# Kernel optimization log

Hardware: AMD Instinct MI355X
Metric: run time of the kernel (lower is better)

Reference implementation:

```python
import jax, jax.numpy as jnp
import numpy as np

NB_HEAD = 16
SIZE_PER_HEAD = 64
D_MODEL = 1024
OUT_DIM = NB_HEAD * SIZE_PER_HEAD
BIG_NEG = 1e10


def setup_inputs() -> dict:
    key = jax.random.key(0)
    ks = jax.random.split(key, 6)
    B, L = 2, 2048
    q = jax.random.normal(ks[0], (B, L, D_MODEL), dtype=jnp.float32)
    k = jax.random.normal(ks[1], (B, L, D_MODEL), dtype=jnp.float32)
    v = jax.random.normal(ks[2], (B, L, D_MODEL), dtype=jnp.float32)
    v_mask = jnp.ones((B, L), dtype=jnp.float32)
    q_mask = jnp.ones((B, L), dtype=jnp.float32)
    # glorot_normal-ish init for the three projection kernels
    std = (2.0 / (D_MODEL + OUT_DIM)) ** 0.5
    q_kernel = jax.random.normal(ks[3], (D_MODEL, OUT_DIM), dtype=jnp.float32) * std
    k_kernel = jax.random.normal(ks[4], (D_MODEL, OUT_DIM), dtype=jnp.float32) * std
    v_kernel = jax.random.normal(ks[5], (D_MODEL, OUT_DIM), dtype=jnp.float32) * std
    return {"q": q, "k": k, "v": v, "v_mask": v_mask, "q_mask": q_mask,
            "q_kernel": q_kernel, "k_kernel": k_kernel, "v_kernel": v_kernel}


def reference(q, k, v, v_mask, q_mask, q_kernel, k_kernel, v_kernel):
    B, Lq, _ = q.shape
    Lk = k.shape[1]
    H, D = NB_HEAD, SIZE_PER_HEAD
    # projections -> [B, L, H, D]
    qw = (q @ q_kernel).reshape(B, Lq, H, D)
    kw = (k @ k_kernel).reshape(B, Lk, H, D)
    vw = (v @ v_kernel).reshape(B, Lk, H, D)
    # scaled dot-product scores [B, H, Lq, Lk]
    scores = jnp.einsum('bqhd,bkhd->bhqk', qw, kw) / jnp.sqrt(jnp.float32(D))
    # additive key mask (original permutes so mask broadcasts over key axis)
    scores = scores - (1.0 - v_mask)[:, None, None, :] * BIG_NEG
    a = jax.nn.softmax(scores, axis=-1)
    # weighted sum -> [B, Lq, H, D] -> [B, Lq, H*D]
    o = jnp.einsum('bhqk,bkhd->bqhd', a, vw).reshape(B, Lq, H * D)
    # multiplicative query mask on output
    o = o * q_mask[:, :, None]
    return o
```

## Files before the change

kernel.cpp:

```cpp
#include <hip/hip_runtime.h>
#include <hip/hip_bf16.h>

#define B_SZ 2
#define SEQ  2048
#define DM   1024
#define NH   16
#define HD   64

typedef __attribute__((ext_vector_type(8))) short bf16x8;
typedef __attribute__((ext_vector_type(4))) short bf16x4;
typedef __attribute__((ext_vector_type(4))) float f32x4;
typedef __attribute__((ext_vector_type(16))) float f32x16;

__device__ __forceinline__ short f2b(float f) {
    __hip_bfloat16 h = __float2bfloat16(f);
    return *reinterpret_cast<short*>(&h);
}

__device__ __forceinline__ void async_copy16(void* lds, const void* g) {
    __builtin_amdgcn_global_load_lds(
        (const __attribute__((address_space(1))) void*)g,
        (__attribute__((address_space(3))) void*)lds, 16, 0, 0);
}

__global__ __launch_bounds__(256) void kPre(
    const float* __restrict__ q, const float* __restrict__ k, const float* __restrict__ v,
    const float* __restrict__ w0, const float* __restrict__ w1, const float* __restrict__ w2,
    short* __restrict__ qb, short* __restrict__ kb, short* __restrict__ vb,
    short* __restrict__ t0, short* __restrict__ t1, short* __restrict__ t2) {
    int z = blockIdx.z, tid = threadIdx.x;
    if (z < 3) {
        const float* src = z == 0 ? q : (z == 1 ? k : v);
        short*       dst = z == 0 ? qb : (z == 1 ? kb : vb);
        size_t i = ((size_t)blockIdx.x * 256 + tid) * 8;
        float4 a0 = *reinterpret_cast<const float4*>(src + i);
        float4 a1 = *reinterpret_cast<const float4*>(src + i + 4);
        bf16x8 c;
        c[0] = f2b(a0.x); c[1] = f2b(a0.y); c[2] = f2b(a0.z); c[3] = f2b(a0.w);
        c[4] = f2b(a1.x); c[5] = f2b(a1.y); c[6] = f2b(a1.z); c[7] = f2b(a1.w);
        *reinterpret_cast<bf16x8*>(dst + i) = c;
    } else {
        if (blockIdx.x >= 256) return;
        const float* w = z == 3 ? w0 : (z == 4 ? w1 : w2);
        short*       t = z == 3 ? t0 : (z == 4 ? t1 : t2);
        __shared__ float tile[64][65];
        int n0 = (blockIdx.x & 15) * 64, k0 = (blockIdx.x >> 4) * 64;
        int c = tid & 63, rr = tid >> 6;
#pragma unroll
        for (int i = 0; i < 16; i++) {
            int kk = i * 4 + rr;
            tile[kk][c] = w[(size_t)(k0 + kk) * DM + n0 + c];
        }
        __syncthreads();
#pragma unroll
        for (int i = 0; i < 16; i++) {
            int nn = i * 4 + rr;
            t[(size_t)(n0 + nn) * DM + k0 + c] = f2b(tile[c][nn]);
        }
    }
}

__global__ __launch_bounds__(256) void kProj(
    const short* __restrict__ qb, const short* __restrict__ kb, const short* __restrict__ vb,
    const short* __restrict__ wtq, const short* __restrict__ wtk, const short* __restrict__ wtv,
    short* __restrict__ qw, short* __restrict__ kw, short* __restrict__ vwT) {
    int z = blockIdx.z;
    const short* A  = z == 0 ? qb : (z == 1 ? kb : vb);
    const short* Bt = z == 0 ? wtq : (z == 1 ? wtk : wtv);

    __shared__ short As[128 * 64];
    __shared__ short Bs[128 * 64];

    int tid = threadIdx.x;
    int m0 = blockIdx.y * 128, n0 = blockIdx.x * 128;
    int wv = tid >> 6, lane = tid & 63, quad = lane >> 4, ln = lane & 15;
    int rblk = (wv >> 1) * 64, cblk = (wv & 1) * 64;

    int rA = wv * 32;
    int srow = rA + (lane >> 3), scol = (lane & 7) * 8;

    f32x4 zero = {0.f, 0.f, 0.f, 0.f};
    f32x4 acc[4][4];
#pragma unroll
    for (int rt = 0; rt < 4; rt++)
#pragma unroll
        for (int ct = 0; ct < 4; ct++) acc[rt][ct] = zero;

    for (int ks = 0; ks < DM; ks += 64) {
        const short* gA = A  + (size_t)(m0 + srow) * DM + ks + scol;
        const short* gB = Bt + (size_t)(n0 + srow) * DM + ks + scol;
#pragma unroll
        for (int i = 0; i < 4; i++) {
            async_copy16(&As[(rA + i * 8) * 64], gA + (size_t)i * 8 * DM);
            async_copy16(&Bs[(rA + i * 8) * 64], gB + (size_t)i * 8 * DM);
        }
        __syncthreads();
#pragma unroll
        for (int kc = 0; kc < 2; kc++) {
            bf16x8 af[4], bfv[4];
#pragma unroll
            for (int rt = 0; rt < 4; rt++)
                af[rt] = *reinterpret_cast<bf16x8*>(&As[(rblk + rt * 16 + ln) * 64 + kc * 32 + quad * 8]);
#pragma unroll
            for (int ct = 0; ct < 4; ct++)
                bfv[ct] = *reinterpret_cast<bf16x8*>(&Bs[(cblk + ct * 16 + ln) * 64 + kc * 32 + quad * 8]);
#pragma unroll
            for (int rt = 0; rt < 4; rt++)
#pragma unroll
                for (int ct = 0; ct < 4; ct++)
                    acc[rt][ct] = __builtin_amdgcn_mfma_f32_16x16x32_bf16(
                        af[rt], bfv[ct], acc[rt][ct], 0, 0, 0);
        }
        __syncthreads();
    }

    if (z < 2) {
        short* C = z == 0 ? qw : kw;
#pragma unroll
        for (int rt = 0; rt < 4; rt++)
#pragma unroll
            for (int r = 0; r < 4; r++) {
                int row = m0 + rblk + rt * 16 + quad * 4 + r;
#pragma unroll
                for (int ct = 0; ct < 4; ct++)
                    C[(size_t)row * DM + n0 + cblk + ct * 16 + ln] = f2b(acc[rt][ct][r]);
            }
    } else {
#pragma unroll
        for (int rt = 0; rt < 4; rt++) {
            int srow0 = m0 + rblk + rt * 16 + quad * 4;
            int bb = srow0 >> 11, lk = srow0 & (SEQ - 1);
#pragma unroll
            for (int ct = 0; ct < 4; ct++) {
                int coln = n0 + cblk + ct * 16 + ln;
                int hh = coln >> 6, dd = coln & 63;
                bf16x4 pk;
                pk[0] = f2b(acc[rt][ct][0]); pk[1] = f2b(acc[rt][ct][1]);
                pk[2] = f2b(acc[rt][ct][2]); pk[3] = f2b(acc[rt][ct][3]);
                *reinterpret_cast<bf16x4*>(
                    &vwT[(((size_t)bb * NH + hh) * HD + dd) * SEQ + lk]) = pk;
            }
        }
    }
}

__global__ __launch_bounds__(256, 2) void kAttn(
    const short* __restrict__ qw, const short* __restrict__ kw, const short* __restrict__ vwT,
    const float* __restrict__ vmask, const float* __restrict__ qmask, float* __restrict__ out) {
    int b = blockIdx.z, h = blockIdx.y, lq0 = blockIdx.x * 128;
    int tid = threadIdx.x, wv = tid >> 6, lane = tid & 63;
    int l5 = lane & 31, half = lane >> 5;

    __shared__ short Ks[128][72];
    __shared__ short Vt[64][136];
    __shared__ short Ps[4][32][136];

    const short* qrow = qw + (size_t)(b * SEQ + lq0 + wv * 32 + l5) * DM + h * HD;
    bf16x8 qf[4];
#pragma unroll
    for (int ki = 0; ki < 4; ki++)
        qf[ki] = *reinterpret_cast<const bf16x8*>(qrow + ki * 16 + half * 8);

    float lrow = 0.f;
    f32x16 o0, o1;
#pragma unroll
    for (int i = 0; i < 16; i++) { o0[i] = 0.f; o1[i] = 0.f; }

    int krow = tid >> 1, kcol = (tid & 1) * 32;
    int vrow = tid >> 2, vcol = (tid & 3) * 32;
    const short* kp = kw + (size_t)(b * SEQ + krow) * DM + h * HD + kcol;
    const short* vp = vwT + ((size_t)(b * NH + h) * HD + vrow) * SEQ + vcol;
    const float* vmb = vmask + b * SEQ;

    bf16x8 kr[4], vr[4];
#pragma unroll
    for (int i = 0; i < 4; i++) {
        kr[i] = *reinterpret_cast<const bf16x8*>(kp + i * 8);
        vr[i] = *reinterpret_cast<const bf16x8*>(vp + i * 8);
    }

    for (int it = 0; it < SEQ / 128; it++) {
        int lk0 = it * 128;
#pragma unroll
        for (int i = 0; i < 4; i++) {
            *reinterpret_cast<bf16x8*>(&Ks[krow][kcol + i * 8]) = kr[i];
            *reinterpret_cast<bf16x8*>(&Vt[vrow][vcol + i * 8]) = vr[i];
        }
        __syncthreads();

        if (it + 1 < SEQ / 128) {
            kp += (size_t)128 * DM;
            vp += 128;
#pragma unroll
            for (int i = 0; i < 4; i++) {
                kr[i] = *reinterpret_cast<const bf16x8*>(kp + i * 8);
                vr[i] = *reinterpret_cast<const bf16x8*>(vp + i * 8);
            }
        }

        f32x16 s[4];
#pragma unroll
        for (int lt = 0; lt < 4; lt++)
#pragma unroll
            for (int i = 0; i < 16; i++) s[lt][i] = 0.f;
#pragma unroll
        for (int lt = 0; lt < 4; lt++)
#pragma unroll
            for (int ki = 0; ki < 4; ki++) {
                bf16x8 kf = *reinterpret_cast<bf16x8*>(&Ks[lt * 32 + l5][ki * 16 + half * 8]);
                s[lt] = __builtin_amdgcn_mfma_f32_32x32x16_bf16(kf, qf[ki], s[lt], 0, 0, 0);
            }

        float rs = 0.f;
#pragma unroll
        for (int lt = 0; lt < 4; lt++)
#pragma unroll
            for (int g = 0; g < 4; g++) {
                float4 mv = *reinterpret_cast<const float4*>(
                    &vmb[lk0 + lt * 32 + 8 * g + 4 * half]);
                float p0 = __expf(s[lt][4 * g + 0] * 0.125f - (1.0f - mv.x) * 1e10f);
                float p1 = __expf(s[lt][4 * g + 1] * 0.125f - (1.0f - mv.y) * 1e10f);
                float p2 = __expf(s[lt][4 * g + 2] * 0.125f - (1.0f - mv.z) * 1e10f);
                float p3 = __expf(s[lt][4 * g + 3] * 0.125f - (1.0f - mv.w) * 1e10f);
                rs += (p0 + p1) + (p2 + p3);
                bf16x4 pk;
                pk[0] = f2b(p0); pk[1] = f2b(p1); pk[2] = f2b(p2); pk[3] = f2b(p3);
                *reinterpret_cast<bf16x4*>(&Ps[wv][l5][lt * 32 + 8 * g + 4 * half]) = pk;
            }
        rs += __shfl_xor(rs, 32);
        lrow += rs;

        bf16x8 pf[8];
#pragma unroll
        for (int ki = 0; ki < 8; ki++)
            pf[ki] = *reinterpret_cast<bf16x8*>(&Ps[wv][l5][ki * 16 + half * 8]);

#pragma unroll
        for (int ki = 0; ki < 8; ki++) {
            bf16x8 vf0 = *reinterpret_cast<bf16x8*>(&Vt[l5][ki * 16 + half * 8]);
            bf16x8 vf1 = *reinterpret_cast<bf16x8*>(&Vt[32 + l5][ki * 16 + half * 8]);
            o0 = __builtin_amdgcn_mfma_f32_32x32x16_bf16(vf0, pf[ki], o0, 0, 0, 0);
            o1 = __builtin_amdgcn_mfma_f32_32x32x16_bf16(vf1, pf[ki], o1, 0, 0, 0);
        }
        __syncthreads();
    }

    int lq = lq0 + wv * 32 + l5;
    float sc2 = (1.0f / lrow) * qmask[b * SEQ + lq];
    float* orow = out + (size_t)(b * SEQ + lq) * DM + h * HD;
#pragma unroll
    for (int g = 0; g < 4; g++) {
        float4 st0, st1;
        st0.x = o0[4 * g + 0] * sc2; st0.y = o0[4 * g + 1] * sc2;
        st0.z = o0[4 * g + 2] * sc2; st0.w = o0[4 * g + 3] * sc2;
        st1.x = o1[4 * g + 0] * sc2; st1.y = o1[4 * g + 1] * sc2;
        st1.z = o1[4 * g + 2] * sc2; st1.w = o1[4 * g + 3] * sc2;
        *reinterpret_cast<float4*>(&orow[8 * g + 4 * half]) = st0;
        *reinterpret_cast<float4*>(&orow[32 + 8 * g + 4 * half]) = st1;
    }
}

extern "C" void kernel_launch(void* const* d_in, const int* in_sizes, int n_in,
                              void* d_out, int out_size, void* d_ws, size_t ws_size,
                              hipStream_t stream) {
    const float* q  = (const float*)d_in[0];
    const float* k  = (const float*)d_in[1];
    const float* v  = (const float*)d_in[2];
    const float* vm = (const float*)d_in[3];
    const float* qm = (const float*)d_in[4];
    const float* qk = (const float*)d_in[5];
    const float* kk = (const float*)d_in[6];
    const float* vk = (const float*)d_in[7];
    float* out = (float*)d_out;

    short* ws  = (short*)d_ws;
    short* wtq = ws;
    short* wtk = wtq + 1024 * 1024;
    short* wtv = wtk + 1024 * 1024;
    short* vb  = wtv + 1024 * 1024;
    short* qw  = vb + (size_t)4096 * 1024;
    short* kw  = qw + (size_t)4096 * 1024;
    short* vwT = kw + (size_t)4096 * 1024;
    short* qb = (short*)d_out;
    short* kb = qb + (size_t)4096 * 1024;

    kPre <<<dim3(2048, 1, 6), 256, 0, stream>>>(q, k, v, qk, kk, vk,
                                                qb, kb, vb, wtq, wtk, wtv);
    kProj<<<dim3(8, 32, 3), 256, 0, stream>>>(qb, kb, vb, wtq, wtk, wtv, qw, kw, vwT);
    kAttn<<<dim3(16, 16, 2), 256, 0, stream>>>(qw, kw, vwT, vm, qm, out);
}
```

Before: 232.8 us.

## Keep attention probabilities in registers via lane shuffles instead of LDS round-trip

Result: slower. 238.4 us (+2.4%).

```diff
diff --git a/kernel.cpp b/kernel.cpp
--- a/kernel.cpp
+++ b/kernel.cpp
@@ -15,6 +15,12 @@
 __device__ __forceinline__ short f2b(float f) {
     __hip_bfloat16 h = __float2bfloat16(f);
     return *reinterpret_cast<short*>(&h);
+}
+
+__device__ __forceinline__ int cvtpk(float a, float b) {
+    int r;
+    asm("v_cvt_pk_bf16_f32 %0, %1, %2" : "=v"(r) : "v"(a), "v"(b));
+    return r;
 }
 
 __device__ __forceinline__ void async_copy16(void* lds, const void* g) {
@@ -144,7 +150,7 @@
     }
 }
 
-__global__ __launch_bounds__(256, 2) void kAttn(
+__global__ __launch_bounds__(256, 3) void kAttn(
     const short* __restrict__ qw, const short* __restrict__ kw, const short* __restrict__ vwT,
     const float* __restrict__ vmask, const float* __restrict__ qmask, float* __restrict__ out) {
     int b = blockIdx.z, h = blockIdx.y, lq0 = blockIdx.x * 128;
@@ -153,7 +159,6 @@
 
     __shared__ short Ks[128][72];
     __shared__ short Vt[64][136];
-    __shared__ short Ps[4][32][136];
 
     const short* qrow = qw + (size_t)(b * SEQ + lq0 + wv * 32 + l5) * DM + h * HD;
     bf16x8 qf[4];
@@ -172,6 +177,9 @@
     const short* vp = vwT + ((size_t)(b * NH + h) * HD + vrow) * SEQ + vcol;
     const float* vmb = vmask + b * SEQ;
 
+    const float C1 = 0.18033688011f;
+    const float C2 = 1.4426950e10f;
+
     bf16x8 kr[4], vr[4];
 #pragma unroll
     for (int i = 0; i < 4; i++) {
@@ -198,50 +206,59 @@
             }
         }
 
-        f32x16 s[4];
-#pragma unroll
-        for (int lt = 0; lt < 4; lt++)
-#pragma unroll
-            for (int i = 0; i < 16; i++) s[lt][i] = 0.f;
-#pragma unroll
-        for (int lt = 0; lt < 4; lt++)
+        float rs = 0.f;
+#pragma unroll
+        for (int lt = 0; lt < 4; lt++) {
+            f32x16 s;
+#pragma unroll
+            for (int i = 0; i < 16; i++) s[i] = 0.f;
 #pragma unroll
             for (int ki = 0; ki < 4; ki++) {
                 bf16x8 kf = *reinterpret_cast<bf16x8*>(&Ks[lt * 32 + l5][ki * 16 + half * 8]);
-                s[lt] = __builtin_amdgcn_mfma_f32_32x32x16_bf16(kf, qf[ki], s[lt], 0, 0, 0);
-            }
-
-        float rs = 0.f;
-#pragma unroll
-        for (int lt = 0; lt < 4; lt++)
+                s = __builtin_amdgcn_mfma_f32_32x32x16_bf16(kf, qf[ki], s, 0, 0, 0);
+            }
+
+            float p[16];
 #pragma unroll
             for (int g = 0; g < 4; g++) {
                 float4 mv = *reinterpret_cast<const float4*>(
                     &vmb[lk0 + lt * 32 + 8 * g + 4 * half]);
-                float p0 = __expf(s[lt][4 * g + 0] * 0.125f - (1.0f - mv.x) * 1e10f);
-                float p1 = __expf(s[lt][4 * g + 1] * 0.125f - (1.0f - mv.y) * 1e10f);
-                float p2 = __expf(s[lt][4 * g + 2] * 0.125f - (1.0f - mv.z) * 1e10f);
-                float p3 = __expf(s[lt][4 * g + 3] * 0.125f - (1.0f - mv.w) * 1e10f);
+                float p0 = __builtin_amdgcn_exp2f(fmaf(s[4 * g + 0], C1, fmaf(mv.x, C2, -C2)));
+                float p1 = __builtin_amdgcn_exp2f(fmaf(s[4 * g + 1], C1, fmaf(mv.y, C2, -C2)));
+                float p2 = __builtin_amdgcn_exp2f(fmaf(s[4 * g + 2], C1, fmaf(mv.z, C2, -C2)));
+                float p3 = __builtin_amdgcn_exp2f(fmaf(s[4 * g + 3], C1, fmaf(mv.w, C2, -C2)));
                 rs += (p0 + p1) + (p2 + p3);
-                bf16x4 pk;
-                pk[0] = f2b(p0); pk[1] = f2b(p1); pk[2] = f2b(p2); pk[3] = f2b(p3);
-                *reinterpret_cast<bf16x4*>(&Ps[wv][l5][lt * 32 + 8 * g + 4 * half]) = pk;
-            }
+                p[4 * g + 0] = p0; p[4 * g + 1] = p1;
+                p[4 * g + 2] = p2; p[4 * g + 3] = p3;
+            }
+
+            int wA = cvtpk(p[0],  p[1]),  wB = cvtpk(p[2],  p[3]);
+            int wC = cvtpk(p[4],  p[5]),  wD = cvtpk(p[6],  p[7]);
+            int wE = cvtpk(p[8],  p[9]),  wF = cvtpk(p[10], p[11]);
+            int wG = cvtpk(p[12], p[13]), wH = cvtpk(p[14], p[15]);
+            int xA = __shfl_xor(wA, 32), xB = __shfl_xor(wB, 32);
+            int xC = __shfl_xor(wC, 32), xD = __shfl_xor(wD, 32);
+            int xE = __shfl_xor(wE, 32), xF = __shfl_xor(wF, 32);
+            int xG = __shfl_xor(wG, 32), xH = __shfl_xor(wH, 32);
+            bool lo = (half == 0);
+            union { int i[4]; bf16x8 v; } uA, uB;
+            uA.i[0] = lo ? wA : xC; uA.i[1] = lo ? wB : xD;
+            uA.i[2] = lo ? xA : wC; uA.i[3] = lo ? xB : wD;
+            uB.i[0] = lo ? wE : xG; uB.i[1] = lo ? wF : xH;
+            uB.i[2] = lo ? xE : wG; uB.i[3] = lo ? xF : wH;
+
+            bf16x8 vf00 = *reinterpret_cast<bf16x8*>(&Vt[l5]     [(2 * lt) * 16 + half * 8]);
+            bf16x8 vf01 = *reinterpret_cast<bf16x8*>(&Vt[32 + l5][(2 * lt) * 16 + half * 8]);
+            bf16x8 vf10 = *reinterpret_cast<bf16x8*>(&Vt[l5]     [(2 * lt + 1) * 16 + half * 8]);
+            bf16x8 vf11 = *reinterpret_cast<bf16x8*>(&Vt[32 + l5][(2 * lt + 1) * 16 + half * 8]);
+            o0 = __builtin_amdgcn_mfma_f32_32x32x16_bf16(vf00, uA.v, o0, 0, 0, 0);
+            o1 = __builtin_amdgcn_mfma_f32_32x32x16_bf16(vf01, uA.v, o1, 0, 0, 0);
+            o0 = __builtin_amdgcn_mfma_f32_32x32x16_bf16(vf10, uB.v, o0, 0, 0, 0);
+            o1 = __builtin_amdgcn_mfma_f32_32x32x16_bf16(vf11, uB.v, o1, 0, 0, 0);
+        }
+
         rs += __shfl_xor(rs, 32);
         lrow += rs;
-
-        bf16x8 pf[8];
-#pragma unroll
-        for (int ki = 0; ki < 8; ki++)
-            pf[ki] = *reinterpret_cast<bf16x8*>(&Ps[wv][l5][ki * 16 + half * 8]);
-
-#pragma unroll
-        for (int ki = 0; ki < 8; ki++) {
-            bf16x8 vf0 = *reinterpret_cast<bf16x8*>(&Vt[l5][ki * 16 + half * 8]);
-            bf16x8 vf1 = *reinterpret_cast<bf16x8*>(&Vt[32 + l5][ki * 16 + half * 8]);
-            o0 = __builtin_amdgcn_mfma_f32_32x32x16_bf16(vf0, pf[ki], o0, 0, 0, 0);
-            o1 = __builtin_amdgcn_mfma_f32_32x32x16_bf16(vf1, pf[ki], o1, 0, 0, 0);
-        }
         __syncthreads();
     }
 
```
